# Kernel tuning notes

Measured on AMD Instinct MI355X. Metric: run time of the kernel, lower is better.

The kernel has to match this reference:

```python
import jax, jax.numpy as jnp
import numpy as np

T, B, H, C = 4096, 32, 512, 32000

def setup_inputs() -> dict:
    key = jax.random.key(0)
    k1, k2, k3, k4, k5 = jax.random.split(key, 5)
    decoder_output = jax.random.normal(k1, (T, B, H), dtype=jnp.float32)
    align_w = jax.random.normal(k2, (H,), dtype=jnp.float32) * (1.0 / np.sqrt(H))
    align_b = jax.random.normal(k3, (), dtype=jnp.float32) * 0.01
    out_w = jax.random.normal(k4, (C, H), dtype=jnp.float32) * (1.0 / np.sqrt(H))
    out_b = jax.random.normal(k5, (C,), dtype=jnp.float32) * 0.01
    return {"decoder_output": decoder_output, "align_w": align_w,
            "align_b": align_b, "out_w": out_w, "out_b": out_b}

def reference(decoder_output, align_w, align_b, out_w, out_b):
    # e[b,t] = tanh(align(decoder_output[t,b]))  -- vectorized over (t,b)
    e = jnp.tanh(jnp.einsum('tbh,h->bt', decoder_output, align_w) + align_b)  # [B,T]
    alpha = jax.nn.softmax(e, axis=-1)                                        # [B,T]
    context = jnp.einsum('bt,tbh->bh', alpha, decoder_output)                 # [B,H]
    return context @ out_w.T + out_b                                          # [B,C]
```

## Files before the change

kernel.cpp:

```cpp
#include <hip/hip_runtime.h>
#include <hip/hip_bf16.h>
#include <math.h>

#define TT 4096
#define BB 32
#define HH 512
#define CC 32000
#define NCHUNK 64
#define TPC 64
#define HQ 4
#define K3_TC 128
#define OSLICE (BB*CC)
#define OW_PAD 36

#define WS_CTX    0
#define WS_LPART  16384
#define WS_BIG    18432

__device__ __forceinline__ float dot4(const float4 a, const float4 b) {
  return fmaf(a.w, b.w, fmaf(a.z, b.z, fmaf(a.y, b.y, fmaf(a.x, b.x, 0.f))));
}

__global__ __launch_bounds__(256) void k1_partials(
    const float* __restrict__ dec, const float* __restrict__ aw,
    const float* __restrict__ abp,
    float* __restrict__ ctx_part, float* __restrict__ l_part)
{
  const int chunk = blockIdx.x;
  const int b     = blockIdx.y;
  const int tid   = threadIdx.x;
  const int wv = tid >> 6, ln = tid & 63;
  const float ab = abp[0];
  const float4 aw0 = *(const float4*)(aw + ln*4);
  const float4 aw1 = *(const float4*)(aw + 256 + ln*4);

  const size_t rowstep = (size_t)BB*HH;
  const float* base = dec + ((size_t)(chunk*TPC + wv*16)*BB + b)*HH + (size_t)ln*4;

  float4 c0 = make_float4(0.f,0.f,0.f,0.f), c1 = make_float4(0.f,0.f,0.f,0.f);
  float l = 0.f;

  for (int it = 0; it < 16; it += 2) {
    const float* p0 = base + (size_t)it*rowstep;
    const float* p1 = base + (size_t)(it+1)*rowstep;
    const float4 xa0 = *(const float4*)(p0);
    const float4 xa1 = *(const float4*)(p0 + 256);
    const float4 xb0 = *(const float4*)(p1);
    const float4 xb1 = *(const float4*)(p1 + 256);
    float da = dot4(xa0, aw0) + dot4(xa1, aw1);
    float db = dot4(xb0, aw0) + dot4(xb1, aw1);
    #pragma unroll
    for (int off = 32; off > 0; off >>= 1) {
      da += __shfl_xor(da, off);
      db += __shfl_xor(db, off);
    }
    const float exa = __expf(2.f*(da + ab));
    const float exb = __expf(2.f*(db + ab));
    const float tha = 1.f - 2.f*__builtin_amdgcn_rcpf(exa + 1.f);
    const float thb = 1.f - 2.f*__builtin_amdgcn_rcpf(exb + 1.f);
    const float wa = __expf(tha);
    const float wb = __expf(thb);
    l += wa + wb;
    c0.x = fmaf(wa, xa0.x, fmaf(wb, xb0.x, c0.x));
    c0.y = fmaf(wa, xa0.y, fmaf(wb, xb0.y, c0.y));
    c0.z = fmaf(wa, xa0.z, fmaf(wb, xb0.z, c0.z));
    c0.w = fmaf(wa, xa0.w, fmaf(wb, xb0.w, c0.w));
    c1.x = fmaf(wa, xa1.x, fmaf(wb, xb1.x, c1.x));
    c1.y = fmaf(wa, xa1.y, fmaf(wb, xb1.y, c1.y));
    c1.z = fmaf(wa, xa1.z, fmaf(wb, xb1.z, c1.z));
    c1.w = fmaf(wa, xa1.w, fmaf(wb, xb1.w, c1.w));
  }

  __shared__ float s_ctx[4][HH];
  __shared__ float s_l[4];
  *(float4*)&s_ctx[wv][ln*4]       = c0;
  *(float4*)&s_ctx[wv][256 + ln*4] = c1;
  if (ln == 0) s_l[wv] = l;
  __syncthreads();
  if (tid < 128) {
    const int h = tid * 4;
    float4 a = make_float4(0.f,0.f,0.f,0.f);
    #pragma unroll
    for (int w2 = 0; w2 < 4; ++w2) {
      const float4 v = *(const float4*)&s_ctx[w2][h];
      a.x += v.x; a.y += v.y; a.z += v.z; a.w += v.w;
    }
    const size_t pp = (size_t)b*NCHUNK + chunk;
    *(float4*)(ctx_part + pp*HH + h) = a;
    if (tid == 0) l_part[pp] = s_l[0] + s_l[1] + s_l[2] + s_l[3];
  }
}

__global__ __launch_bounds__(256) void k2_combine(
    const float* __restrict__ ctx_part, const float* __restrict__ l_part,
    float* __restrict__ ctx)
{
  const int b = blockIdx.x;
  const int tid = threadIdx.x;
  const int half = tid >> 7, hf = tid & 127;
  const int h = hf * 4;

  float4 a = make_float4(0.f,0.f,0.f,0.f);
  const float* basep = ctx_part + ((size_t)b*NCHUNK + half*32)*HH + h;
  #pragma unroll 8
  for (int p = 0; p < 32; ++p) {
    const float4 v = *(const float4*)(basep + (size_t)p*HH);
    a.x += v.x; a.y += v.y; a.z += v.z; a.w += v.w;
  }

  __shared__ float4 s_part[2][128];
  __shared__ float s_L;
  s_part[half][hf] = a;
  if (tid < 64) {
    float Lv = l_part[b*NCHUNK + tid];
    #pragma unroll
    for (int off = 32; off > 0; off >>= 1) Lv += __shfl_xor(Lv, off);
    if (tid == 0) s_L = Lv;
  }
  __syncthreads();
  if (tid < 128) {
    const float4 r0 = s_part[0][tid];
    const float4 r1 = s_part[1][tid];
    const float inv = 1.f / s_L;
    *(float4*)(ctx + (size_t)b*HH + tid*4) = make_float4(
        (r0.x+r1.x)*inv, (r0.y+r1.y)*inv, (r0.z+r1.z)*inv, (r0.w+r1.w)*inv);
  }
}

__global__ __launch_bounds__(256) void k3_matmul(
    const float* __restrict__ ctx, const float* __restrict__ ow,
    float* __restrict__ out_part)
{
  __shared__ float s_ow[K3_TC*OW_PAD];
  __shared__ float s_cx[32*128];
  const int tid = threadIdx.x;
  const int ci = tid & 63, wv = tid >> 6;
  const int cblk = blockIdx.x, hq = blockIdx.y;
  const int h0 = hq * 128;
  const int crow0 = cblk * K3_TC;

  #pragma unroll
  for (int rep = 0; rep < 4; ++rep) {
    const int j = rep*1024 + tid*4;
    const int b = j >> 7, hh = j & 127;
    *(float4*)&s_cx[j] = *(const float4*)(ctx + (size_t)b*HH + h0 + hh);
  }

  float acc[2][8];
  #pragma unroll
  for (int g = 0; g < 2; ++g)
    #pragma unroll
    for (int bi = 0; bi < 8; ++bi) acc[g][bi] = 0.f;

  for (int ch = 0; ch < 4; ++ch) {
    if (ch) __syncthreads();
    #pragma unroll
    for (int r2 = 0; r2 < 4; ++r2) {
      const int j = r2*256 + tid;
      const int r = j >> 3, hp = j & 7;
      *(float4*)&s_ow[r*OW_PAD + hp*4] =
          *(const float4*)(ow + (size_t)(crow0 + r)*HH + h0 + ch*32 + hp*4);
    }
    __syncthreads();
    #pragma unroll
    for (int s = 0; s < 8; ++s) {
      float4 w4[2];
      #pragma unroll
      for (int g = 0; g < 2; ++g)
        w4[g] = *(const float4*)&s_ow[(g*64 + ci)*OW_PAD + s*4];
      #pragma unroll
      for (int bi = 0; bi < 8; ++bi) {
        const float4 c4 = *(const float4*)&s_cx[(wv*8 + bi)*128 + ch*32 + s*4];
        #pragma unroll
        for (int g = 0; g < 2; ++g) {
          acc[g][bi] = fmaf(w4[g].w, c4.w, fmaf(w4[g].z, c4.z,
                       fmaf(w4[g].y, c4.y, fmaf(w4[g].x, c4.x, acc[g][bi]))));
        }
      }
    }
  }

  float* op = out_part + (size_t)hq*OSLICE;
  #pragma unroll
  for (int bi = 0; bi < 8; ++bi) {
    #pragma unroll
    for (int g = 0; g < 2; ++g)
      op[(size_t)(wv*8 + bi)*CC + crow0 + g*64 + ci] = acc[g][bi];
  }
}

__global__ __launch_bounds__(256) void k4_final(
    const float* __restrict__ out_part, const float* __restrict__ ob,
    float* __restrict__ out)
{
  const size_t i = ((size_t)blockIdx.x * 256 + threadIdx.x) * 4;
  float4 r = *(const float4*)(out_part + i);
  #pragma unroll
  for (int q = 1; q < HQ; ++q) {
    const float4 p = *(const float4*)(out_part + (size_t)q*OSLICE + i);
    r.x += p.x; r.y += p.y; r.z += p.z; r.w += p.w;
  }
  const int cIdx = (int)(i % CC);
  const float4 b4 = *(const float4*)(ob + cIdx);
  *(float4*)(out + i) = make_float4(r.x+b4.x, r.y+b4.y, r.z+b4.z, r.w+b4.w);
}

extern "C" void kernel_launch(void* const* d_in, const int* in_sizes, int n_in,
                              void* d_out, int out_size, void* d_ws, size_t ws_size,
                              hipStream_t stream) {
  const float* dec = (const float*)d_in[0];
  const float* aw  = (const float*)d_in[1];
  const float* ab  = (const float*)d_in[2];
  const float* ow  = (const float*)d_in[3];
  const float* ob  = (const float*)d_in[4];
  float* out = (float*)d_out;
  float* ws  = (float*)d_ws;
  float* ctx   = ws + WS_CTX;
  float* lpart = ws + WS_LPART;
  float* big   = ws + WS_BIG;

  k1_partials<<<dim3(NCHUNK, BB), 256, 0, stream>>>(dec, aw, ab, big, lpart);
  k2_combine<<<dim3(BB), 256, 0, stream>>>(big, lpart, ctx);
  k3_matmul<<<dim3(CC/K3_TC, HQ), 256, 0, stream>>>(ctx, ow, big);
  k4_final<<<dim3((BB*CC)/(256*4)), 256, 0, stream>>>(big, ob, out);
}
```

Measured before the change: 90.76 us.

## Double-buffer out_w tiles in k3 via direct global-to-LDS loads with XOR swizzle

The matmul kernel now streams out_w tiles straight into LDS with global_load_lds, skipping the register round trip. Two LDS buffers let the load of the next h-chunk run while the current one is computed. The padded layout is replaced by an XOR swizzle on the column index to avoid bank conflicts. The cost is twice the LDS for the weight tile, which may lower occupancy, plus reliance on a hardware-specific builtin and manual vmcnt waits.

New measurement: 109.3 us. 20.5% more time.

```diff
diff --git a/kernel.cpp b/kernel.cpp
--- a/kernel.cpp
+++ b/kernel.cpp
@@ -11,11 +11,14 @@
 #define HQ 4
 #define K3_TC 128
 #define OSLICE (BB*CC)
-#define OW_PAD 36
 
 #define WS_CTX    0
 #define WS_LPART  16384
 #define WS_BIG    18432
+
+#define GLOAD_LDS(g, l) \
+  __builtin_amdgcn_global_load_lds((const __attribute__((address_space(1))) void*)(g), \
+                                   (__attribute__((address_space(3))) void*)(l), 16, 0, 0)
 
 __device__ __forceinline__ float dot4(const float4 a, const float4 b) {
   return fmaf(a.w, b.w, fmaf(a.z, b.z, fmaf(a.y, b.y, fmaf(a.x, b.x, 0.f))));
@@ -131,10 +134,10 @@
     const float* __restrict__ ctx, const float* __restrict__ ow,
     float* __restrict__ out_part)
 {
-  __shared__ float s_ow[K3_TC*OW_PAD];
+  __shared__ float s_ow[2][K3_TC*32];
   __shared__ float s_cx[32*128];
   const int tid = threadIdx.x;
-  const int ci = tid & 63, wv = tid >> 6;
+  const int ci = tid & 63, wv = tid >> 6, ln = tid & 63;
   const int cblk = blockIdx.x, hq = blockIdx.y;
   const int h0 = hq * 128;
   const int crow0 = cblk * K3_TC;
@@ -146,6 +149,22 @@
     *(float4*)&s_cx[j] = *(const float4*)(ctx + (size_t)b*HH + h0 + hh);
   }
 
+  auto ISSUE = [&](int ch, int bf) {
+    const float* gbase = ow + (size_t)crow0*HH + h0 + ch*32;
+    #pragma unroll
+    for (int i2 = 0; i2 < 4; ++i2) {
+      const int i = wv*4 + i2;
+      const int j = i*64 + ln;
+      const int r = j >> 3;
+      const int hp4 = (j & 7) ^ (r & 7);
+      GLOAD_LDS(gbase + (size_t)r*HH + hp4*4, &s_ow[bf][i*256]);
+    }
+  };
+
+  ISSUE(0, 0);
+  asm volatile("s_waitcnt vmcnt(0)" ::: "memory");
+  __syncthreads();
+
   float acc[2][8];
   #pragma unroll
   for (int g = 0; g < 2; ++g)
@@ -153,21 +172,16 @@
     for (int bi = 0; bi < 8; ++bi) acc[g][bi] = 0.f;
 
   for (int ch = 0; ch < 4; ++ch) {
-    if (ch) __syncthreads();
-    #pragma unroll
-    for (int r2 = 0; r2 < 4; ++r2) {
-      const int j = r2*256 + tid;
-      const int r = j >> 3, hp = j & 7;
-      *(float4*)&s_ow[r*OW_PAD + hp*4] =
-          *(const float4*)(ow + (size_t)(crow0 + r)*HH + h0 + ch*32 + hp*4);
-    }
-    __syncthreads();
+    const int bf = ch & 1;
+    if (ch < 3) ISSUE(ch+1, bf^1);
     #pragma unroll
     for (int s = 0; s < 8; ++s) {
       float4 w4[2];
       #pragma unroll
-      for (int g = 0; g < 2; ++g)
-        w4[g] = *(const float4*)&s_ow[(g*64 + ci)*OW_PAD + s*4];
+      for (int g = 0; g < 2; ++g) {
+        const int row = g*64 + ci;
+        w4[g] = *(const float4*)&s_ow[bf][(row*8 + (s ^ (ci & 7))) * 4];
+      }
       #pragma unroll
       for (int bi = 0; bi < 8; ++bi) {
         const float4 c4 = *(const float4*)&s_cx[(wv*8 + bi)*128 + ch*32 + s*4];
@@ -177,6 +191,10 @@
                        fmaf(w4[g].y, c4.y, fmaf(w4[g].x, c4.x, acc[g][bi]))));
         }
       }
+    }
+    if (ch < 3) {
+      asm volatile("s_waitcnt vmcnt(0)" ::: "memory");
+      __syncthreads();
     }
   }
 
```
